# Kernel optimization log

Hardware: AMD Instinct MI355X
Metric: run time of the kernel (lower is better)

The kernel has to match this reference:

```python
import jax, jax.numpy as jnp
import numpy as np

N, E, G = 50000, 1000000, 128          # nodes, edges, graphs
NODE_DIM, EDGE_DIM, HID, EMB = 8, 3, 32, 64


def setup_inputs() -> dict:
    key = jax.random.key(0)
    ks = list(jax.random.split(key, 16))
    def nrm(k, shape, s=1.0):
        return jax.random.normal(k, shape, dtype=jnp.float32) * s
    return {
        "x": nrm(ks[0], (N, NODE_DIM)),
        "edge_attr": nrm(ks[1], (E, EDGE_DIM)),
        "the_ratios": jax.random.uniform(ks[2], (5,), dtype=jnp.float32),
        "edge_index": jax.random.randint(ks[3], (2, E), 0, N),
        "batch": jnp.sort(jax.random.randint(ks[4], (N,), 0, G)),
        "the_ids": jax.random.randint(ks[5], (5,), 0, 118),
        # edge_nn: Linear(3,32) -> ReLU -> Linear(32, 8*32)
        "W1": nrm(ks[6], (EDGE_DIM, 32), 0.3), "b1": jnp.zeros((32,), jnp.float32),
        "W2": nrm(ks[7], (32, NODE_DIM * HID), 0.1), "b2": jnp.zeros((NODE_DIM * HID,), jnp.float32),
        "emb": nrm(ks[8], (118, EMB), 0.1),
        # NNConv root weight + bias
        "root": nrm(ks[9], (NODE_DIM, HID), 0.3), "conv_bias": jnp.zeros((HID,), jnp.float32),
        "fc0_w": nrm(ks[10], (HID + EMB, 64), 0.1), "fc0_b": jnp.zeros((64,), jnp.float32),
        "fc1_w": nrm(ks[11], (64, 32), 0.1), "fc1_b": jnp.zeros((32,), jnp.float32),
        "fc2_w": nrm(ks[12], (32, 1), 0.1), "fc2_b": jnp.zeros((1,), jnp.float32),
    }


def reference(x, edge_attr, the_ratios, edge_index, batch, the_ids,
              W1, b1, W2, b2, emb, root, conv_bias,
              fc0_w, fc0_b, fc1_w, fc1_b, fc2_w, fc2_b):
    src, dst = edge_index[0], edge_index[1]
    # per-edge weight matrix from edge MLP: [E, NODE_DIM, HID]
    h = jax.nn.relu(edge_attr @ W1 + b1)
    We = (h @ W2 + b2).reshape(E, NODE_DIM, HID)
    # gather source node feats, per-edge matmul: [E, HID]
    msg = jnp.einsum('ei,eio->eo', x[src], We)
    # scatter-mean to target nodes
    s = jax.ops.segment_sum(msg, dst, num_segments=N)
    cnt = jax.ops.segment_sum(jnp.ones((E,), msg.dtype), dst, num_segments=N)
    agg = s / jnp.maximum(cnt, 1.0)[:, None]
    # NNConv root transform + bias, then ReLU
    h_node = jax.nn.relu(x @ root + agg + conv_bias)
    # global mean pool over graphs
    gs = jax.ops.segment_sum(h_node, batch, num_segments=G)
    gc = jax.ops.segment_sum(jnp.ones((N,), h_node.dtype), batch, num_segments=G)
    pooled = gs / jnp.maximum(gc, 1.0)[:, None]
    # weighted element embedding, broadcast to all graphs
    u = jnp.sum(emb[the_ids] * the_ratios[:, None], axis=0)
    z = jnp.concatenate([pooled, jnp.broadcast_to(u, (G, EMB))], axis=1)
    z = jax.nn.relu(z @ fc0_w + fc0_b)
    z = jax.nn.relu(z @ fc1_w + fc1_b)
    return z @ fc2_w + fc2_b
```

## Files before the change

### kernel.cpp

```cpp
#include <hip/hip_runtime.h>

#define NODE_DIM 8

typedef __attribute__((ext_vector_type(8))) short short8;
typedef __attribute__((ext_vector_type(4))) float f32x4;

#define DOT8(xv, WT) ((xv)[0]*(WT)[0] + (xv)[1]*(WT)[1] + (xv)[2]*(WT)[2] + (xv)[3]*(WT)[3] + \
                      (xv)[4]*(WT)[4] + (xv)[5]*(WT)[5] + (xv)[6]*(WT)[6] + (xv)[7]*(WT)[7])

static __device__ __forceinline__ unsigned pk_bf16(float a, float b) {
    unsigned ua = __float_as_uint(a), ub = __float_as_uint(b);
    ua = (ua + 0x7fffu + ((ua >> 16) & 1u)) >> 16;
    ub = (ub + 0x7fffu + ((ub >> 16) & 1u)) & 0xffff0000u;
    return (ua & 0xffffu) | ub;
}

__global__ __launch_bounds__(256)
void edge_kernel(const float* __restrict__ x,
                 const float* __restrict__ ea,
                 const int* __restrict__ eidx,
                 const float* __restrict__ W1, const float* __restrict__ b1,
                 const float* __restrict__ W2, const float* __restrict__ b2,
                 float* __restrict__ s, int* __restrict__ cnt,
                 int E)
{
    __shared__ __align__(16) short lds_b[18 * 64 * 8];

    const int t = threadIdx.x;

    for (int f = t; f < 18 * 64 * 8; f += 256) {
        const int j   = f & 7;
        const int ln  = (f >> 3) & 63;
        const int fid = f >> 9;
        const int kk  = fid >> 1, ot = fid & 1;
        const int qq  = ln >> 4, ol = ln & 15;
        float v;
        if (kk < 8) v = W2[(kk * 4 + qq) * 256 + j * 32 + ot * 16 + ol];
        else        v = (qq == 0) ? b2[j * 32 + ot * 16 + ol] : 0.f;
        unsigned uv = __float_as_uint(v);
        uv = (uv + 0x7fffu + ((uv >> 16) & 1u)) >> 16;
        lds_b[f] = (short)uv;
    }
    __syncthreads();

    const int lane = t & 63;
    const int e_l  = lane & 15;
    const int q    = lane >> 4;

    float w10[8], w11[8], w12[8], b1r[8];
#pragma unroll
    for (int t2 = 0; t2 < 8; ++t2) {
        const int k = 4 * t2 + q;
        w10[t2] = W1[k]; w11[t2] = W1[32 + k]; w12[t2] = W1[64 + k]; b1r[t2] = b1[k];
    }

    const int wave = blockIdx.x * 4 + (t >> 6);
    const int nwav = gridDim.x * 4;
    const int ngrp = (E + 15) / 16;

    for (int grp = wave; grp < ngrp; grp += nwav) {
        const int base = grp * 16;
        int ej = base + e_l; if (ej >= E) ej = E - 1;
        const int src = eidx[ej];
        const int dst = eidx[E + ej];
        const float ea0 = ea[3 * ej], ea1 = ea[3 * ej + 1], ea2 = ea[3 * ej + 2];
        const float4 xa = *(const float4*)(x + (size_t)(unsigned)src * 8);
        const float4 xb = *(const float4*)(x + (size_t)(unsigned)src * 8 + 4);
        const float xr[8] = {xa.x, xa.y, xa.z, xa.w, xb.x, xb.y, xb.z, xb.w};

        float h[8];
#pragma unroll
        for (int t2 = 0; t2 < 8; ++t2) {
            const float z = b1r[t2] + ea0 * w10[t2] + ea1 * w11[t2] + ea2 * w12[t2];
            h[t2] = z > 0.f ? z : 0.f;
        }

        f32x4 acc0 = {0.f, 0.f, 0.f, 0.f};
        f32x4 acc1 = {0.f, 0.f, 0.f, 0.f};

#pragma unroll
        for (int kk = 0; kk < 9; ++kk) {
            const float hk = (kk < 8) ? h[kk] : 1.f;
            union { short8 v; unsigned u[4]; } af;
#pragma unroll
            for (int p = 0; p < 4; ++p)
                af.u[p] = pk_bf16(hk * xr[2 * p], hk * xr[2 * p + 1]);
            const short8 bf0 = *(const short8*)&lds_b[((kk * 2 + 0) * 64 + lane) * 8];
            const short8 bf1 = *(const short8*)&lds_b[((kk * 2 + 1) * 64 + lane) * 8];
            acc0 = __builtin_amdgcn_mfma_f32_16x16x32_bf16(af.v, bf0, acc0, 0, 0, 0);
            acc1 = __builtin_amdgcn_mfma_f32_16x16x32_bf16(af.v, bf1, acc1, 0, 0, 0);
        }

#pragma unroll
        for (int r = 0; r < 4; ++r) {
            const int m  = q * 4 + r;
            const int eg = base + m;
            const int dr = __shfl(dst, m, 16);
            if (eg < E) {
                atomicAdd(&s[(size_t)(unsigned)dr * 32 + e_l],      acc0[r]);
                atomicAdd(&s[(size_t)(unsigned)dr * 32 + 16 + e_l], acc1[r]);
            }
        }
        if (lane < 16 && base + e_l < E) atomicAdd(&cnt[dst], 1);
    }
}

__global__ __launch_bounds__(256)
void node_pool_kernel(const float* __restrict__ s,
                      const int* __restrict__ cnt,
                      const float* __restrict__ x,
                      const float* __restrict__ root,
                      const float* __restrict__ conv_bias,
                      const int* __restrict__ batch,
                      float* __restrict__ gsum, int N)
{
    __shared__ float red[256];
    const int t    = threadIdx.x;
    const int o    = t & 31;
    const int slot = t >> 5;
    const int base = blockIdx.x * 8;
    const int n    = base + slot;

    float rootr[8];
#pragma unroll
    for (int i = 0; i < 8; ++i) rootr[i] = root[i * 32 + o];
    const float cb = conv_bias[o];

    float v = 0.f;
    int   b = 0;
    if (n < N) {
        b = batch[n];
        const int   c    = cnt[n];
        const float rinv = 1.f / (float)(c > 1 ? c : 1);
        const float* xp  = x + (size_t)n * 8;
        float xv[8];
#pragma unroll
        for (int i = 0; i < 8; ++i) xv[i] = xp[i];
        const float t2 = s[(size_t)n * 32 + o] * rinv + cb + DOT8(xv, rootr);
        v = t2 > 0.f ? t2 : 0.f;
    }

    const int nlast  = (base + 7 < N) ? base + 7 : N - 1;
    const int bfirst = batch[base];
    const int blast  = batch[nlast];

    if (bfirst == blast && base + 7 < N) {
        red[t] = v;
        __syncthreads();
        if (t < 32) {
            float p = 0.f;
#pragma unroll
            for (int c2 = 0; c2 < 8; ++c2) p += red[t + 32 * c2];
            atomicAdd(&gsum[bfirst * 32 + t], p);
        }
    } else {
        if (n < N) atomicAdd(&gsum[b * 32 + o], v);
    }
}

__global__ __launch_bounds__(128)
void mlp_kernel(const float* __restrict__ gsum,
                const int* __restrict__ batch,
                const float* __restrict__ ratios,
                const int* __restrict__ ids,
                const float* __restrict__ emb,
                const float* __restrict__ fc0w, const float* __restrict__ fc0b,
                const float* __restrict__ fc1w, const float* __restrict__ fc1b,
                const float* __restrict__ fc2w, const float* __restrict__ fc2b,
                float* __restrict__ out, int N)
{
    __shared__ float zs[96];
    __shared__ float z1[64];
    __shared__ float z2[32];
    __shared__ int seg[2];

    const int g = blockIdx.x;
    const int t = threadIdx.x;

    if (t < 2) {
        const int target = g + t;
        int lo = 0, hi = N;
        while (lo < hi) {
            const int mid = (lo + hi) >> 1;
            if (batch[mid] < target) lo = mid + 1; else hi = mid;
        }
        seg[t] = lo;
    }
    __syncthreads();

    float c = (float)(seg[1] - seg[0]);
    if (c < 1.f) c = 1.f;

    if (t < 32) zs[t] = gsum[g * 32 + t] / c;
    if (t >= 32 && t < 96) {
        const int j = t - 32;
        float u = 0.f;
#pragma unroll
        for (int r = 0; r < 5; ++r) u += ratios[r] * emb[(size_t)ids[r] * 64 + j];
        zs[32 + j] = u;
    }
    __syncthreads();

    if (t < 64) {
        float a = fc0b[t];
        for (int k = 0; k < 96; ++k) a += zs[k] * fc0w[k * 64 + t];
        z1[t] = a > 0.f ? a : 0.f;
    }
    __syncthreads();

    if (t < 32) {
        float a = fc1b[t];
        for (int k = 0; k < 64; ++k) a += z1[k] * fc1w[k * 32 + t];
        z2[t] = a > 0.f ? a : 0.f;
    }
    __syncthreads();

    if (t == 0) {
        float a = fc2b[0];
        for (int k = 0; k < 32; ++k) a += z2[k] * fc2w[k];
        out[g] = a;
    }
}

extern "C" void kernel_launch(void* const* d_in, const int* in_sizes, int n_in,
                              void* d_out, int out_size, void* d_ws, size_t ws_size,
                              hipStream_t stream)
{
    const float* x         = (const float*)d_in[0];
    const float* ea        = (const float*)d_in[1];
    const float* ratios    = (const float*)d_in[2];
    const int*   eidx      = (const int*)  d_in[3];
    const int*   batch     = (const int*)  d_in[4];
    const int*   ids       = (const int*)  d_in[5];
    const float* W1        = (const float*)d_in[6];
    const float* b1        = (const float*)d_in[7];
    const float* W2        = (const float*)d_in[8];
    const float* b2        = (const float*)d_in[9];
    const float* emb       = (const float*)d_in[10];
    const float* root      = (const float*)d_in[11];
    const float* conv_bias = (const float*)d_in[12];
    const float* fc0w      = (const float*)d_in[13];
    const float* fc0b      = (const float*)d_in[14];
    const float* fc1w      = (const float*)d_in[15];
    const float* fc1b      = (const float*)d_in[16];
    const float* fc2w      = (const float*)d_in[17];
    const float* fc2b      = (const float*)d_in[18];

    const int N = in_sizes[0] / NODE_DIM;
    const int E = in_sizes[1] / 3;
    const int G = out_size;

    float* s    = (float*)d_ws;
    int*   cnt  = (int*)((char*)d_ws + (size_t)N * 32 * 4);
    float* gsum = (float*)((char*)d_ws + (size_t)N * 32 * 4 + (size_t)N * 4);
    (void)hipMemsetAsync(d_ws, 0, (size_t)N * 32 * 4 + (size_t)N * 4 + (size_t)G * 32 * 4, stream);

    edge_kernel<<<2048, 256, 0, stream>>>(x, ea, eidx, W1, b1, W2, b2, s, cnt, E);
    node_pool_kernel<<<(N + 7) / 8, 256, 0, stream>>>(s, cnt, x, root, conv_bias,
                                                      batch, gsum, N);
    mlp_kernel<<<G, 128, 0, stream>>>(gsum, batch, ratios, ids, emb,
                                      fc0w, fc0b, fc1w, fc1b, fc2w, fc2b,
                                      (float*)d_out, N);
}
```

Baseline: 280.3 us.

## Process two edge groups per wave iteration with hardware bf16 conversion

The edge loop now handles two 16-edge groups per iteration, so the gathers, MFMAs and atomics of two independent groups can interleave and hide latency. Software bf16 rounding is replaced by the v_cvt_pk_bf16_f32 instruction. The bias row (kk=8) is computed from x alone instead of multiplying by 1, and launch bounds now request 4 blocks per CU. The cost is higher register pressure, which the occupancy hint may force into spills.

```diff
diff --git a/kernel.cpp b/kernel.cpp
--- a/kernel.cpp
+++ b/kernel.cpp
@@ -8,14 +8,13 @@
 #define DOT8(xv, WT) ((xv)[0]*(WT)[0] + (xv)[1]*(WT)[1] + (xv)[2]*(WT)[2] + (xv)[3]*(WT)[3] + \
                       (xv)[4]*(WT)[4] + (xv)[5]*(WT)[5] + (xv)[6]*(WT)[6] + (xv)[7]*(WT)[7])
 
-static __device__ __forceinline__ unsigned pk_bf16(float a, float b) {
-    unsigned ua = __float_as_uint(a), ub = __float_as_uint(b);
-    ua = (ua + 0x7fffu + ((ua >> 16) & 1u)) >> 16;
-    ub = (ub + 0x7fffu + ((ub >> 16) & 1u)) & 0xffff0000u;
-    return (ua & 0xffffu) | ub;
-}
-
-__global__ __launch_bounds__(256)
+static __device__ __forceinline__ unsigned cvt_pk_bf16(float a, float b) {
+    unsigned r;
+    asm("v_cvt_pk_bf16_f32 %0, %1, %2" : "=v"(r) : "v"(a), "v"(b));
+    return r;
+}
+
+__global__ __launch_bounds__(256, 4)
 void edge_kernel(const float* __restrict__ x,
                  const float* __restrict__ ea,
                  const int* __restrict__ eidx,
@@ -58,50 +57,91 @@
     const int nwav = gridDim.x * 4;
     const int ngrp = (E + 15) / 16;
 
-    for (int grp = wave; grp < ngrp; grp += nwav) {
-        const int base = grp * 16;
-        int ej = base + e_l; if (ej >= E) ej = E - 1;
-        const int src = eidx[ej];
-        const int dst = eidx[E + ej];
-        const float ea0 = ea[3 * ej], ea1 = ea[3 * ej + 1], ea2 = ea[3 * ej + 2];
-        const float4 xa = *(const float4*)(x + (size_t)(unsigned)src * 8);
-        const float4 xb = *(const float4*)(x + (size_t)(unsigned)src * 8 + 4);
-        const float xr[8] = {xa.x, xa.y, xa.z, xa.w, xb.x, xb.y, xb.z, xb.w};
-
-        float h[8];
+    for (int g0 = 2 * wave; g0 < ngrp; g0 += 2 * nwav) {
+        const bool v1    = (g0 + 1) < ngrp;
+        const int  base0 = g0 * 16;
+        const int  base1 = (v1 ? g0 + 1 : g0) * 16;
+
+        int ej0 = base0 + e_l; if (ej0 >= E) ej0 = E - 1;
+        int ej1 = base1 + e_l; if (ej1 >= E) ej1 = E - 1;
+
+        const int src0 = eidx[ej0];
+        const int dst0 = eidx[E + ej0];
+        const int src1 = eidx[ej1];
+        const int dst1 = eidx[E + ej1];
+        const float ea00 = ea[3 * ej0], ea01 = ea[3 * ej0 + 1], ea02 = ea[3 * ej0 + 2];
+        const float ea10 = ea[3 * ej1], ea11 = ea[3 * ej1 + 1], ea12 = ea[3 * ej1 + 2];
+        const float4 xa0 = *(const float4*)(x + (size_t)(unsigned)src0 * 8);
+        const float4 xb0 = *(const float4*)(x + (size_t)(unsigned)src0 * 8 + 4);
+        const float4 xa1 = *(const float4*)(x + (size_t)(unsigned)src1 * 8);
+        const float4 xb1 = *(const float4*)(x + (size_t)(unsigned)src1 * 8 + 4);
+        const float xr0[8] = {xa0.x, xa0.y, xa0.z, xa0.w, xb0.x, xb0.y, xb0.z, xb0.w};
+        const float xr1[8] = {xa1.x, xa1.y, xa1.z, xa1.w, xb1.x, xb1.y, xb1.z, xb1.w};
+
+        float h0[8], h1[8];
 #pragma unroll
         for (int t2 = 0; t2 < 8; ++t2) {
-            const float z = b1r[t2] + ea0 * w10[t2] + ea1 * w11[t2] + ea2 * w12[t2];
-            h[t2] = z > 0.f ? z : 0.f;
-        }
-
-        f32x4 acc0 = {0.f, 0.f, 0.f, 0.f};
-        f32x4 acc1 = {0.f, 0.f, 0.f, 0.f};
-
-#pragma unroll
-        for (int kk = 0; kk < 9; ++kk) {
-            const float hk = (kk < 8) ? h[kk] : 1.f;
-            union { short8 v; unsigned u[4]; } af;
-#pragma unroll
-            for (int p = 0; p < 4; ++p)
-                af.u[p] = pk_bf16(hk * xr[2 * p], hk * xr[2 * p + 1]);
+            const float z0 = b1r[t2] + ea00 * w10[t2] + ea01 * w11[t2] + ea02 * w12[t2];
+            const float z1 = b1r[t2] + ea10 * w10[t2] + ea11 * w11[t2] + ea12 * w12[t2];
+            h0[t2] = z0 > 0.f ? z0 : 0.f;
+            h1[t2] = z1 > 0.f ? z1 : 0.f;
+        }
+
+        f32x4 a00 = {0.f, 0.f, 0.f, 0.f};
+        f32x4 a01 = {0.f, 0.f, 0.f, 0.f};
+        f32x4 a10 = {0.f, 0.f, 0.f, 0.f};
+        f32x4 a11 = {0.f, 0.f, 0.f, 0.f};
+
+        {
+            union { short8 v; unsigned u[4]; } id0, id1;
+#pragma unroll
+            for (int p = 0; p < 4; ++p) {
+                id0.u[p] = cvt_pk_bf16(xr0[2 * p], xr0[2 * p + 1]);
+                id1.u[p] = cvt_pk_bf16(xr1[2 * p], xr1[2 * p + 1]);
+            }
+            const short8 bf0 = *(const short8*)&lds_b[(16 * 64 + lane) * 8];
+            const short8 bf1 = *(const short8*)&lds_b[(17 * 64 + lane) * 8];
+            a00 = __builtin_amdgcn_mfma_f32_16x16x32_bf16(id0.v, bf0, a00, 0, 0, 0);
+            a01 = __builtin_amdgcn_mfma_f32_16x16x32_bf16(id0.v, bf1, a01, 0, 0, 0);
+            a10 = __builtin_amdgcn_mfma_f32_16x16x32_bf16(id1.v, bf0, a10, 0, 0, 0);
+            a11 = __builtin_amdgcn_mfma_f32_16x16x32_bf16(id1.v, bf1, a11, 0, 0, 0);
+        }
+
+#pragma unroll
+        for (int kk = 0; kk < 8; ++kk) {
             const short8 bf0 = *(const short8*)&lds_b[((kk * 2 + 0) * 64 + lane) * 8];
             const short8 bf1 = *(const short8*)&lds_b[((kk * 2 + 1) * 64 + lane) * 8];
-            acc0 = __builtin_amdgcn_mfma_f32_16x16x32_bf16(af.v, bf0, acc0, 0, 0, 0);
-            acc1 = __builtin_amdgcn_mfma_f32_16x16x32_bf16(af.v, bf1, acc1, 0, 0, 0);
+            const float hk0 = h0[kk], hk1 = h1[kk];
+            union { short8 v; unsigned u[4]; } af0, af1;
+#pragma unroll
+            for (int p = 0; p < 4; ++p) {
+                af0.u[p] = cvt_pk_bf16(hk0 * xr0[2 * p], hk0 * xr0[2 * p + 1]);
+                af1.u[p] = cvt_pk_bf16(hk1 * xr1[2 * p], hk1 * xr1[2 * p + 1]);
+            }
+            a00 = __builtin_amdgcn_mfma_f32_16x16x32_bf16(af0.v, bf0, a00, 0, 0, 0);
+            a01 = __builtin_amdgcn_mfma_f32_16x16x32_bf16(af0.v, bf1, a01, 0, 0, 0);
+            a10 = __builtin_amdgcn_mfma_f32_16x16x32_bf16(af1.v, bf0, a10, 0, 0, 0);
+            a11 = __builtin_amdgcn_mfma_f32_16x16x32_bf16(af1.v, bf1, a11, 0, 0, 0);
         }
 
 #pragma unroll
         for (int r = 0; r < 4; ++r) {
-            const int m  = q * 4 + r;
-            const int eg = base + m;
-            const int dr = __shfl(dst, m, 16);
-            if (eg < E) {
-                atomicAdd(&s[(size_t)(unsigned)dr * 32 + e_l],      acc0[r]);
-                atomicAdd(&s[(size_t)(unsigned)dr * 32 + 16 + e_l], acc1[r]);
+            const int m   = q * 4 + r;
+            const int dr0 = __shfl(dst0, m, 16);
+            const int dr1 = __shfl(dst1, m, 16);
+            if (base0 + m < E) {
+                atomicAdd(&s[(size_t)(unsigned)dr0 * 32 + e_l],      a00[r]);
+                atomicAdd(&s[(size_t)(unsigned)dr0 * 32 + 16 + e_l], a01[r]);
             }
-        }
-        if (lane < 16 && base + e_l < E) atomicAdd(&cnt[dst], 1);
+            if (v1 && base1 + m < E) {
+                atomicAdd(&s[(size_t)(unsigned)dr1 * 32 + e_l],      a10[r]);
+                atomicAdd(&s[(size_t)(unsigned)dr1 * 32 + 16 + e_l], a11[r]);
+            }
+        }
+        if (lane < 16) {
+            if (base0 + e_l < E)       atomicAdd(&cnt[dst0], 1);
+            if (v1 && base1 + e_l < E) atomicAdd(&cnt[dst1], 1);
+        }
     }
 }
 
```

Measured after the change: 272.7 us. 1.03x faster.
